# Performance work log

Measured on AMD Instinct MI355X. Metric: run time of the kernel, lower is better.

Reference implementation:

```python
import jax, jax.numpy as jnp
import numpy as np

K = 16  # FLAGS.num_neighbors
N = 2562  # ellipsoid vertices
B = 4     # FLAGS.batch_size
M = 16384 # points per cloud
D = 3     # coordinate dim


def _mean_neighborhood(coord, pc, k):
    # coord: [N, D] query vertices; pc: [B, D, M] point cloud (channels-first)
    x2 = jnp.sum(coord * coord, axis=1)[None, :, None]          # [1, N, 1]
    y2 = jnp.sum(pc * pc, axis=1)[:, None, :]                   # [B, 1, M]
    xy = jnp.einsum('nd,bdm->bnm', coord, pc)                   # [B, N, M]
    d2 = x2 + y2 - 2.0 * xy                                     # [B, N, M]
    _, idx = jax.lax.top_k(-d2, k)                               # [B, N, K] indices into M
    Y = jnp.transpose(pc, (0, 2, 1))                             # [B, M, D]
    bv = jnp.arange(pc.shape[0])[:, None, None]                  # [B, 1, 1]
    knnY = Y[bv, idx]                                            # [B, N, K, D]
    knnY_mean = jnp.mean(knnY, axis=2)                           # [B, N, D]
    return knnY_mean[0]                                          # [N, D] (matches knnY_mean[0])


def setup_inputs() -> dict:
    key = jax.random.key(0)
    ks = jax.random.split(key, 5)
    inputs = jax.random.normal(ks[0], (N, D), dtype=jnp.float32)
    pcs = [jax.random.normal(ks[i + 1], (B, D, M), dtype=jnp.float32) for i in range(4)]
    return {"inputs": inputs, "pc0": pcs[0], "pc1": pcs[1], "pc2": pcs[2], "pc3": pcs[3]}


def reference(inputs, pc0, pc1, pc2, pc3):
    s0 = _mean_neighborhood(inputs, pc0, K)
    s1 = _mean_neighborhood(inputs, pc1, K)
    s2 = _mean_neighborhood(inputs, pc2, K)
    s3 = _mean_neighborhood(inputs, pc3, K)
    return jnp.concatenate([inputs, s0, s1, s2, s3], axis=1)  # [N, 5*D]
```

## Files before the change

kernel.cpp:

```cpp
#include <hip/hip_runtime.h>
#include <stdint.h>
#include <math.h>

#define NQ    2562
#define MPTS  16384
#define QPB   8
#define NBQ   321
#define NT    (MPTS / 256)
#define CAP   320

__global__ __launch_bounds__(256)
void passthrough_kernel(const float* __restrict__ inp, float* __restrict__ out) {
    int gid = blockIdx.x * 256 + threadIdx.x;
    if (gid < NQ * 3) {
        int n = gid / 3, c = gid - n * 3;
        out[n * 15 + c] = inp[gid];
    }
}

__device__ __forceinline__ float sqsum3(float y0, float y1, float y2) {
    return __fadd_rn(__fadd_rn(__fmul_rn(y0, y0), __fmul_rn(y1, y1)),
                     __fmul_rn(y2, y2));
}
__device__ __forceinline__ float keyf(float xs, float a2, float b2, float c2,
                                      float y0, float y1, float y2, float ysq) {
    float u = fmaf(c2, y2, fmaf(b2, y1, __fmul_rn(a2, y0)));
    return __fsub_rn(__fadd_rn(xs, ysq), u);
}
__device__ __forceinline__ unsigned long long packkey(float k, int m) {
    uint32_t kb = __float_as_uint(k);
    kb ^= (uint32_t)((int32_t)kb >> 31) | 0x80000000u;
    return ((unsigned long long)kb << 32) | (unsigned)m;
}
__device__ __forceinline__ float unmapkey(unsigned long long pk) {
    uint32_t kb = (uint32_t)(pk >> 32);
    return __uint_as_float((kb & 0x80000000u) ? (kb ^ 0x80000000u) : ~kb);
}
__device__ __forceinline__ int prefix_lt(unsigned long long m) {
    return __builtin_amdgcn_mbcnt_hi((unsigned)(m >> 32),
           __builtin_amdgcn_mbcnt_lo((unsigned)m, 0u));
}

__device__ __forceinline__ unsigned long long sort64(unsigned long long v, int lane) {
#pragma unroll
    for (int k = 2; k <= 64; k <<= 1) {
#pragma unroll
        for (int j = k >> 1; j > 0; j >>= 1) {
            unsigned long long p = __shfl_xor(v, j);
            bool up = ((lane & k) == 0) == ((lane & j) == 0);
            bool sw = up ? (p < v) : (v < p);
            v = sw ? p : v;
        }
    }
    return v;
}

__device__ __forceinline__ float rebuild_q(unsigned long long* t16p,
                                           unsigned long long* S, int& cnt,
                                           int lane, bool fin) {
    int c = cnt;
    int full = c >> 6, rem = c & 63;
    int rounds = full + ((fin && rem) ? 1 : 0);
    unsigned long long v = ~0ULL;
    for (int rd = 0; rd < rounds; ++rd) {
        int i = (rd << 6) + lane;
        unsigned long long pk = (i < c) ? S[i] : ~0ULL;
        pk = sort64(pk, lane);
        unsigned long long bsw = __shfl(pk, (31 - lane) & 63);
        v = (lane < 16) ? t16p[lane & 15] : (lane < 32) ? bsw : ~0ULL;
#pragma unroll
        for (int j = 16; j > 0; j >>= 1) {
            unsigned long long p2 = __shfl_xor(v, j);
            bool keepmin = (lane & j) == 0;
            bool less = p2 < v;
            v = (keepmin == less) ? p2 : v;
        }
        if (lane < 16) t16p[lane] = v;
    }
    if (!fin) {
        if (lane < rem) S[lane] = S[(full << 6) + lane];
        cnt = rem;
    } else {
        cnt = 0;
    }
    return unmapkey(__shfl(v, 15));
}

__global__ __launch_bounds__(256)
void knn_kernel(const float* __restrict__ inp,
                const float* __restrict__ pc0, const float* __restrict__ pc1,
                const float* __restrict__ pc2, const float* __restrict__ pc3,
                float* __restrict__ out) {
    const int b    = blockIdx.x;
    const int wid  = threadIdx.x >> 6;
    const int lane = threadIdx.x & 63;

    const int pc = b / NBQ;
    const int nb = b - pc * NBQ;
    const float* __restrict__ P = (pc == 0) ? pc0 : (pc == 1) ? pc1
                                : (pc == 2) ? pc2 : pc3;

    __shared__ unsigned long long stk_sh[4][2][CAP];
    __shared__ unsigned long long t16_sh[4][2][16];

    if (lane < 32) t16_sh[wid][lane >> 4][lane & 15] = ~0ULL;

    float A2[2], B2[2], C2[2], XS[2];
#pragma unroll
    for (int r = 0; r < 2; ++r) {
        int n = QPB * nb + 2 * wid + r;
        n = (n < NQ) ? n : (NQ - 1);
        float x0 = inp[n * 3 + 0];
        float x1 = inp[n * 3 + 1];
        float x2 = inp[n * 3 + 2];
        A2[r] = 2.0f * x0;
        B2[r] = 2.0f * x1;
        C2[r] = 2.0f * x2;
        XS[r] = sqsum3(x0, x1, x2);
    }
    float tau[2];
    int   cnt[2] = {0, 0};

    const float* __restrict__ Pl = P + (lane << 2);

    auto push_tile = [&](int r, int mofs, float k0, float k1, float k2, float k3) {
        unsigned long long b0 = __ballot(k0 <= tau[r]);
        unsigned long long b1 = __ballot(k1 <= tau[r]);
        unsigned long long b2 = __ballot(k2 <= tau[r]);
        unsigned long long b3 = __ballot(k3 <= tau[r]);
        int pre = prefix_lt(b0) + prefix_lt(b1) + prefix_lt(b2) + prefix_lt(b3);
        int tot = __popcll(b0) + __popcll(b1) + __popcll(b2) + __popcll(b3);
        int pos = cnt[r] + pre;
        unsigned long long* S = stk_sh[wid][r];
        if (k0 <= tau[r]) S[pos++] = packkey(k0, mofs + 0);
        if (k1 <= tau[r]) S[pos++] = packkey(k1, mofs + 1);
        if (k2 <= tau[r]) S[pos++] = packkey(k2, mofs + 2);
        if (k3 <= tau[r]) S[pos++] = packkey(k3, mofs + 3);
        cnt[r] += tot;
        if (cnt[r] >= 64)
            tau[r] = rebuild_q(t16_sh[wid][r], S, cnt[r], lane, false);
    };

    {
        float4 ax = *(const float4*)(Pl);
        float4 ay = *(const float4*)(Pl + MPTS);
        float4 az = *(const float4*)(Pl + 2 * MPTS);
        float q0 = sqsum3(ax.x, ay.x, az.x);
        float q1 = sqsum3(ax.y, ay.y, az.y);
        float q2 = sqsum3(ax.z, ay.z, az.z);
        float q3 = sqsum3(ax.w, ay.w, az.w);
#pragma unroll
        for (int r = 0; r < 2; ++r) {
            float k0 = keyf(XS[r], A2[r], B2[r], C2[r], ax.x, ay.x, az.x, q0);
            float k1 = keyf(XS[r], A2[r], B2[r], C2[r], ax.y, ay.y, az.y, q1);
            float k2 = keyf(XS[r], A2[r], B2[r], C2[r], ax.z, ay.z, az.z, q2);
            float k3 = keyf(XS[r], A2[r], B2[r], C2[r], ax.w, ay.w, az.w, q3);
            float km = fminf(fminf(k0, k1), fminf(k2, k3));
            float g = km;
            g = fminf(g, __shfl_xor(g, 1));
            g = fminf(g, __shfl_xor(g, 2));
            float m = g;
            m = fmaxf(m, __shfl_xor(m, 4));
            m = fmaxf(m, __shfl_xor(m, 8));
            m = fmaxf(m, __shfl_xor(m, 16));
            m = fmaxf(m, __shfl_xor(m, 32));
            tau[r] = m;
            push_tile(r, lane << 2, k0, k1, k2, k3);
        }
    }

    float4 cx = *(const float4*)(Pl + 256);
    float4 cy = *(const float4*)(Pl + MPTS + 256);
    float4 cz = *(const float4*)(Pl + 2 * MPTS + 256);

    for (int t = 1; t < NT; ++t) {
        const int tn = (t + 1 < NT) ? t + 1 : t;
        float4 nx = *(const float4*)(Pl + (tn << 8));
        float4 ny = *(const float4*)(Pl + MPTS + (tn << 8));
        float4 nz = *(const float4*)(Pl + 2 * MPTS + (tn << 8));

        const int mofs = (t << 8) + (lane << 2);
        float q0 = sqsum3(cx.x, cy.x, cz.x);
        float q1 = sqsum3(cx.y, cy.y, cz.y);
        float q2 = sqsum3(cx.z, cy.z, cz.z);
        float q3 = sqsum3(cx.w, cy.w, cz.w);
#pragma unroll
        for (int r = 0; r < 2; ++r) {
            float k0 = keyf(XS[r], A2[r], B2[r], C2[r], cx.x, cy.x, cz.x, q0);
            float k1 = keyf(XS[r], A2[r], B2[r], C2[r], cx.y, cy.y, cz.y, q1);
            float k2 = keyf(XS[r], A2[r], B2[r], C2[r], cx.z, cy.z, cz.z, q2);
            float k3 = keyf(XS[r], A2[r], B2[r], C2[r], cx.w, cy.w, cz.w, q3);
            float km = fminf(fminf(k0, k1), fminf(k2, k3));
            if (__ballot(km <= tau[r]))
                push_tile(r, mofs, k0, k1, k2, k3);
        }
        cx = nx; cy = ny; cz = nz;
    }

#pragma unroll
    for (int r = 0; r < 2; ++r) {
        if (cnt[r] > 0)
            rebuild_q(t16_sh[wid][r], stk_sh[wid][r], cnt[r], lane, true);
    }

    {
        const int h   = lane >> 5;
        const int l32 = lane & 31;
        if (l32 < 16) {
            unsigned long long v = t16_sh[wid][h][l32];
            int idx = (int)(unsigned)v;
            float gx = P[idx];
            float gy = P[MPTS + idx];
            float gz = P[2 * MPTS + idx];
#pragma unroll
            for (int off = 8; off > 0; off >>= 1) {
                gx += __shfl_down(gx, off, 16);
                gy += __shfl_down(gy, off, 16);
                gz += __shfl_down(gz, off, 16);
            }
            if (l32 == 0) {
                int n = QPB * nb + 2 * wid + h;
                n = (n < NQ) ? n : (NQ - 1);
                float* o = out + n * 15 + 3 + 3 * pc;
                o[0] = gx * 0.0625f;
                o[1] = gy * 0.0625f;
                o[2] = gz * 0.0625f;
            }
        }
    }
}

extern "C" void kernel_launch(void* const* d_in, const int* in_sizes, int n_in,
                              void* d_out, int out_size, void* d_ws, size_t ws_size,
                              hipStream_t stream) {
    const float* inp = (const float*)d_in[0];
    const float* pc0 = (const float*)d_in[1];
    const float* pc1 = (const float*)d_in[2];
    const float* pc2 = (const float*)d_in[3];
    const float* pc3 = (const float*)d_in[4];
    float* out = (float*)d_out;

    hipLaunchKernelGGL(passthrough_kernel, dim3((NQ * 3 + 255) / 256), dim3(256),
                       0, stream, inp, out);

    hipLaunchKernelGGL(knn_kernel, dim3(4 * NBQ), dim3(256), 0, stream,
                       inp, pc0, pc1, pc2, pc3, out);
}
```

Baseline: 109.2 us.

## Use one query per wave and precompute point squared norms in workspace

Each wave now handles a single query instead of two, which doubles the block count (QPB 8→4, NBQ 641) to raise parallelism and halves per-wave register and shared-memory state. A separate kernel precomputes ||y||^2 for every point into the workspace, and the KNN kernel loads it as a fourth float4 stream instead of recomputing it. The cost is that each point tile is now read by twice as many waves with less reuse per load, plus an extra kernel launch and extra memory traffic for the ysq array.

```diff
diff --git a/kernel.cpp b/kernel.cpp
--- a/kernel.cpp
+++ b/kernel.cpp
@@ -4,8 +4,8 @@
 
 #define NQ    2562
 #define MPTS  16384
-#define QPB   8
-#define NBQ   321
+#define QPB   4
+#define NBQ   641
 #define NT    (MPTS / 256)
 #define CAP   320
 
@@ -87,9 +87,21 @@
 }
 
 __global__ __launch_bounds__(256)
+void ysq_kernel(const float* __restrict__ pc0, const float* __restrict__ pc1,
+                const float* __restrict__ pc2, const float* __restrict__ pc3,
+                float* __restrict__ ysq) {
+    int gid = blockIdx.x * 256 + threadIdx.x;
+    int pc = gid >> 14, m = gid & (MPTS - 1);
+    const float* P = (pc == 0) ? pc0 : (pc == 1) ? pc1 : (pc == 2) ? pc2 : pc3;
+    ysq[gid] = sqsum3(P[m], P[MPTS + m], P[2 * MPTS + m]);
+}
+
+template <bool USE_YSQ>
+__global__ __launch_bounds__(256)
 void knn_kernel(const float* __restrict__ inp,
                 const float* __restrict__ pc0, const float* __restrict__ pc1,
                 const float* __restrict__ pc2, const float* __restrict__ pc3,
+                const float* __restrict__ ysq,
                 float* __restrict__ out) {
     const int b    = blockIdx.x;
     const int wid  = threadIdx.x >> 6;
@@ -100,132 +112,136 @@
     const float* __restrict__ P = (pc == 0) ? pc0 : (pc == 1) ? pc1
                                 : (pc == 2) ? pc2 : pc3;
 
-    __shared__ unsigned long long stk_sh[4][2][CAP];
-    __shared__ unsigned long long t16_sh[4][2][16];
-
-    if (lane < 32) t16_sh[wid][lane >> 4][lane & 15] = ~0ULL;
-
-    float A2[2], B2[2], C2[2], XS[2];
-#pragma unroll
-    for (int r = 0; r < 2; ++r) {
-        int n = QPB * nb + 2 * wid + r;
+    __shared__ unsigned long long stk_sh[4][CAP];
+    __shared__ unsigned long long t16_sh[4][16];
+
+    if (lane < 16) t16_sh[wid][lane] = ~0ULL;
+
+    float A2, B2, C2, XS;
+    {
+        int n = QPB * nb + wid;
         n = (n < NQ) ? n : (NQ - 1);
         float x0 = inp[n * 3 + 0];
         float x1 = inp[n * 3 + 1];
         float x2 = inp[n * 3 + 2];
-        A2[r] = 2.0f * x0;
-        B2[r] = 2.0f * x1;
-        C2[r] = 2.0f * x2;
-        XS[r] = sqsum3(x0, x1, x2);
-    }
-    float tau[2];
-    int   cnt[2] = {0, 0};
+        A2 = 2.0f * x0;
+        B2 = 2.0f * x1;
+        C2 = 2.0f * x2;
+        XS = sqsum3(x0, x1, x2);
+    }
+    float tau;
+    int   cnt = 0;
 
     const float* __restrict__ Pl = P + (lane << 2);
-
-    auto push_tile = [&](int r, int mofs, float k0, float k1, float k2, float k3) {
-        unsigned long long b0 = __ballot(k0 <= tau[r]);
-        unsigned long long b1 = __ballot(k1 <= tau[r]);
-        unsigned long long b2 = __ballot(k2 <= tau[r]);
-        unsigned long long b3 = __ballot(k3 <= tau[r]);
+    const float* __restrict__ Ql = ysq + pc * MPTS + (lane << 2);
+
+    auto push_tile = [&](int mofs, float k0, float k1, float k2, float k3) {
+        unsigned long long b0 = __ballot(k0 <= tau);
+        unsigned long long b1 = __ballot(k1 <= tau);
+        unsigned long long b2 = __ballot(k2 <= tau);
+        unsigned long long b3 = __ballot(k3 <= tau);
         int pre = prefix_lt(b0) + prefix_lt(b1) + prefix_lt(b2) + prefix_lt(b3);
         int tot = __popcll(b0) + __popcll(b1) + __popcll(b2) + __popcll(b3);
-        int pos = cnt[r] + pre;
-        unsigned long long* S = stk_sh[wid][r];
-        if (k0 <= tau[r]) S[pos++] = packkey(k0, mofs + 0);
-        if (k1 <= tau[r]) S[pos++] = packkey(k1, mofs + 1);
-        if (k2 <= tau[r]) S[pos++] = packkey(k2, mofs + 2);
-        if (k3 <= tau[r]) S[pos++] = packkey(k3, mofs + 3);
-        cnt[r] += tot;
-        if (cnt[r] >= 64)
-            tau[r] = rebuild_q(t16_sh[wid][r], S, cnt[r], lane, false);
+        int pos = cnt + pre;
+        unsigned long long* S = stk_sh[wid];
+        if (k0 <= tau) S[pos++] = packkey(k0, mofs + 0);
+        if (k1 <= tau) S[pos++] = packkey(k1, mofs + 1);
+        if (k2 <= tau) S[pos++] = packkey(k2, mofs + 2);
+        if (k3 <= tau) S[pos++] = packkey(k3, mofs + 3);
+        cnt += tot;
+        if (cnt >= 64)
+            tau = rebuild_q(t16_sh[wid], S, cnt, lane, false);
     };
 
     {
         float4 ax = *(const float4*)(Pl);
         float4 ay = *(const float4*)(Pl + MPTS);
         float4 az = *(const float4*)(Pl + 2 * MPTS);
-        float q0 = sqsum3(ax.x, ay.x, az.x);
-        float q1 = sqsum3(ax.y, ay.y, az.y);
-        float q2 = sqsum3(ax.z, ay.z, az.z);
-        float q3 = sqsum3(ax.w, ay.w, az.w);
-#pragma unroll
-        for (int r = 0; r < 2; ++r) {
-            float k0 = keyf(XS[r], A2[r], B2[r], C2[r], ax.x, ay.x, az.x, q0);
-            float k1 = keyf(XS[r], A2[r], B2[r], C2[r], ax.y, ay.y, az.y, q1);
-            float k2 = keyf(XS[r], A2[r], B2[r], C2[r], ax.z, ay.z, az.z, q2);
-            float k3 = keyf(XS[r], A2[r], B2[r], C2[r], ax.w, ay.w, az.w, q3);
-            float km = fminf(fminf(k0, k1), fminf(k2, k3));
-            float g = km;
-            g = fminf(g, __shfl_xor(g, 1));
-            g = fminf(g, __shfl_xor(g, 2));
-            float m = g;
-            m = fmaxf(m, __shfl_xor(m, 4));
-            m = fmaxf(m, __shfl_xor(m, 8));
-            m = fmaxf(m, __shfl_xor(m, 16));
-            m = fmaxf(m, __shfl_xor(m, 32));
-            tau[r] = m;
-            push_tile(r, lane << 2, k0, k1, k2, k3);
-        }
+        float q0, q1, q2, q3;
+        if (USE_YSQ) {
+            float4 aq = *(const float4*)(Ql);
+            q0 = aq.x; q1 = aq.y; q2 = aq.z; q3 = aq.w;
+        } else {
+            q0 = sqsum3(ax.x, ay.x, az.x);
+            q1 = sqsum3(ax.y, ay.y, az.y);
+            q2 = sqsum3(ax.z, ay.z, az.z);
+            q3 = sqsum3(ax.w, ay.w, az.w);
+        }
+        float k0 = keyf(XS, A2, B2, C2, ax.x, ay.x, az.x, q0);
+        float k1 = keyf(XS, A2, B2, C2, ax.y, ay.y, az.y, q1);
+        float k2 = keyf(XS, A2, B2, C2, ax.z, ay.z, az.z, q2);
+        float k3 = keyf(XS, A2, B2, C2, ax.w, ay.w, az.w, q3);
+        float km = fminf(fminf(k0, k1), fminf(k2, k3));
+        float g = km;
+        g = fminf(g, __shfl_xor(g, 1));
+        g = fminf(g, __shfl_xor(g, 2));
+        float m = g;
+        m = fmaxf(m, __shfl_xor(m, 4));
+        m = fmaxf(m, __shfl_xor(m, 8));
+        m = fmaxf(m, __shfl_xor(m, 16));
+        m = fmaxf(m, __shfl_xor(m, 32));
+        tau = m;
+        push_tile(lane << 2, k0, k1, k2, k3);
     }
 
     float4 cx = *(const float4*)(Pl + 256);
     float4 cy = *(const float4*)(Pl + MPTS + 256);
     float4 cz = *(const float4*)(Pl + 2 * MPTS + 256);
+    float4 cq;
+    if (USE_YSQ) cq = *(const float4*)(Ql + 256);
 
     for (int t = 1; t < NT; ++t) {
         const int tn = (t + 1 < NT) ? t + 1 : t;
         float4 nx = *(const float4*)(Pl + (tn << 8));
         float4 ny = *(const float4*)(Pl + MPTS + (tn << 8));
         float4 nz = *(const float4*)(Pl + 2 * MPTS + (tn << 8));
+        float4 nq;
+        if (USE_YSQ) nq = *(const float4*)(Ql + (tn << 8));
 
         const int mofs = (t << 8) + (lane << 2);
-        float q0 = sqsum3(cx.x, cy.x, cz.x);
-        float q1 = sqsum3(cx.y, cy.y, cz.y);
-        float q2 = sqsum3(cx.z, cy.z, cz.z);
-        float q3 = sqsum3(cx.w, cy.w, cz.w);
-#pragma unroll
-        for (int r = 0; r < 2; ++r) {
-            float k0 = keyf(XS[r], A2[r], B2[r], C2[r], cx.x, cy.x, cz.x, q0);
-            float k1 = keyf(XS[r], A2[r], B2[r], C2[r], cx.y, cy.y, cz.y, q1);
-            float k2 = keyf(XS[r], A2[r], B2[r], C2[r], cx.z, cy.z, cz.z, q2);
-            float k3 = keyf(XS[r], A2[r], B2[r], C2[r], cx.w, cy.w, cz.w, q3);
-            float km = fminf(fminf(k0, k1), fminf(k2, k3));
-            if (__ballot(km <= tau[r]))
-                push_tile(r, mofs, k0, k1, k2, k3);
-        }
+        float q0, q1, q2, q3;
+        if (USE_YSQ) {
+            q0 = cq.x; q1 = cq.y; q2 = cq.z; q3 = cq.w;
+        } else {
+            q0 = sqsum3(cx.x, cy.x, cz.x);
+            q1 = sqsum3(cx.y, cy.y, cz.y);
+            q2 = sqsum3(cx.z, cy.z, cz.z);
+            q3 = sqsum3(cx.w, cy.w, cz.w);
+        }
+        float k0 = keyf(XS, A2, B2, C2, cx.x, cy.x, cz.x, q0);
+        float k1 = keyf(XS, A2, B2, C2, cx.y, cy.y, cz.y, q1);
+        float k2 = keyf(XS, A2, B2, C2, cx.z, cy.z, cz.z, q2);
+        float k3 = keyf(XS, A2, B2, C2, cx.w, cy.w, cz.w, q3);
+        float km = fminf(fminf(k0, k1), fminf(k2, k3));
+        if (__ballot(km <= tau))
+            push_tile(mofs, k0, k1, k2, k3);
+
         cx = nx; cy = ny; cz = nz;
-    }
-
-#pragma unroll
-    for (int r = 0; r < 2; ++r) {
-        if (cnt[r] > 0)
-            rebuild_q(t16_sh[wid][r], stk_sh[wid][r], cnt[r], lane, true);
-    }
-
-    {
-        const int h   = lane >> 5;
-        const int l32 = lane & 31;
-        if (l32 < 16) {
-            unsigned long long v = t16_sh[wid][h][l32];
-            int idx = (int)(unsigned)v;
-            float gx = P[idx];
-            float gy = P[MPTS + idx];
-            float gz = P[2 * MPTS + idx];
-#pragma unroll
-            for (int off = 8; off > 0; off >>= 1) {
-                gx += __shfl_down(gx, off, 16);
-                gy += __shfl_down(gy, off, 16);
-                gz += __shfl_down(gz, off, 16);
-            }
-            if (l32 == 0) {
-                int n = QPB * nb + 2 * wid + h;
-                n = (n < NQ) ? n : (NQ - 1);
-                float* o = out + n * 15 + 3 + 3 * pc;
-                o[0] = gx * 0.0625f;
-                o[1] = gy * 0.0625f;
-                o[2] = gz * 0.0625f;
-            }
+        if (USE_YSQ) cq = nq;
+    }
+
+    if (cnt > 0)
+        rebuild_q(t16_sh[wid], stk_sh[wid], cnt, lane, true);
+
+    if (lane < 16) {
+        unsigned long long v = t16_sh[wid][lane];
+        int idx = (int)(unsigned)v;
+        float gx = P[idx];
+        float gy = P[MPTS + idx];
+        float gz = P[2 * MPTS + idx];
+#pragma unroll
+        for (int off = 8; off > 0; off >>= 1) {
+            gx += __shfl_down(gx, off, 16);
+            gy += __shfl_down(gy, off, 16);
+            gz += __shfl_down(gz, off, 16);
+        }
+        if (lane == 0) {
+            int n = QPB * nb + wid;
+            n = (n < NQ) ? n : (NQ - 1);
+            float* o = out + n * 15 + 3 + 3 * pc;
+            o[0] = gx * 0.0625f;
+            o[1] = gy * 0.0625f;
+            o[2] = gz * 0.0625f;
         }
     }
 }
@@ -239,10 +255,19 @@
     const float* pc2 = (const float*)d_in[3];
     const float* pc3 = (const float*)d_in[4];
     float* out = (float*)d_out;
+    float* ysq = (float*)d_ws;
 
     hipLaunchKernelGGL(passthrough_kernel, dim3((NQ * 3 + 255) / 256), dim3(256),
                        0, stream, inp, out);
 
-    hipLaunchKernelGGL(knn_kernel, dim3(4 * NBQ), dim3(256), 0, stream,
-                       inp, pc0, pc1, pc2, pc3, out);
-}
+    const bool use_ysq = (ws_size >= (size_t)(4 * MPTS * sizeof(float)));
+    if (use_ysq) {
+        hipLaunchKernelGGL(ysq_kernel, dim3(4 * MPTS / 256), dim3(256), 0, stream,
+                           pc0, pc1, pc2, pc3, ysq);
+        hipLaunchKernelGGL((knn_kernel<true>), dim3(4 * NBQ), dim3(256), 0, stream,
+                           inp, pc0, pc1, pc2, pc3, ysq, out);
+    } else {
+        hipLaunchKernelGGL((knn_kernel<false>), dim3(4 * NBQ), dim3(256), 0, stream,
+                           inp, pc0, pc1, pc2, pc3, ysq, out);
+    }
+}
```

Measured after the change: 105.6 us. -3.3%, faster.
